# Performance work log

Measured on AMD Instinct MI355X. Metric: run time of the kernel, lower is better.

The kernel has to match this reference:

```python
import jax, jax.numpy as jnp
import numpy as np

MASK_NEG = -1e9

def setup_inputs() -> dict:
    key = jax.random.key(0)
    kq, kk, kv, km = jax.random.split(key, 4)
    B, S, D = 16, 2048, 64
    query = jax.random.normal(kq, (B, S, D), dtype=jnp.float32)
    key_t = jax.random.normal(kk, (B, S, D), dtype=jnp.float32)
    value = jax.random.normal(kv, (B, S, D), dtype=jnp.float32)
    mask = jax.random.randint(km, (B, 1, S), 0, 2, dtype=jnp.int32)
    return {"query": query, "key": key_t, "value": value, "mask": mask}

def reference(query, key, value, mask):
    d = query.shape[-1]
    # scores: [B, S, S]
    scores = jnp.einsum("bqd,bkd->bqk", query, key) / jnp.sqrt(jnp.asarray(d, query.dtype))
    scores = jnp.where(mask == 0, jnp.asarray(MASK_NEG, scores.dtype), scores)
    p_attn = jax.nn.softmax(scores, axis=-1)
    out = jnp.einsum("bqk,bkd->bqd", p_attn, value)
    return out, p_attn
```

## Files before the change

kernel.cpp:

```cpp
#include <hip/hip_runtime.h>
#include <hip/hip_bf16.h>

#define BN 16
#define SN 2048
#define DN 64
#define QB 16
#define NWAVE 8
#define KSEG 256
#define NCH 8

#define SC_L2E 0.18033688011112042f
#define BI_L2E 11.541560327111707f

typedef __attribute__((ext_vector_type(8))) short bf16x8;
typedef __attribute__((ext_vector_type(4))) short bf16x4;
typedef __attribute__((ext_vector_type(4))) float f32x4;
typedef __attribute__((ext_vector_type(4))) int   i32x4;
typedef __attribute__((ext_vector_type(4))) unsigned u32x4;

static __device__ __forceinline__ short f2bf(float f) {
    __hip_bfloat16 h = __float2bfloat16(f);
    union { __hip_bfloat16 h; short s; } u; u.h = h;
    return u.s;
}
static __device__ __forceinline__ float uf(unsigned u) {
    union { unsigned u; float f; } v; v.u = u;
    return v.f;
}
static __device__ __forceinline__ unsigned pk2(float lo, float hi) {
    return ((unsigned)(unsigned short)f2bf(lo)) |
           (((unsigned)(unsigned short)f2bf(hi)) << 16);
}
static __device__ __forceinline__ float fast_exp2(float x) {
#if __has_builtin(__builtin_amdgcn_exp2f)
    return __builtin_amdgcn_exp2f(x);
#else
    return exp2f(x);
#endif
}

__global__ __launch_bounds__(256)
void prep_kv(const float* __restrict__ K, const float* __restrict__ V,
             const int* __restrict__ M,
             short* __restrict__ Kf, short* __restrict__ Vf, float* __restrict__ Mf)
{
    __shared__ short vt[64][72];
    const int b   = blockIdx.x >> 5;
    const int s0  = (blockIdx.x & 31) << 6;
    const int cg0 = s0 >> 5;
    const int tid = threadIdx.x;
    const int sr = tid >> 4;
    const int dc = (tid & 15) << 2;
    #pragma unroll
    for (int i = 0; i < 4; ++i) {
        const int s = sr + i * 16;
        f32x4 vv = *(const f32x4*)(V + ((size_t)b * SN + s0 + s) * DN + dc);
        bf16x4 v4;
        #pragma unroll
        for (int j = 0; j < 4; ++j) v4[j] = f2bf(vv[j]);
        *(bf16x4*)&vt[s][dc] = v4;
    }
    if (tid < 64) {
        const int m = M[(size_t)b * SN + s0 + tid];
        Mf[(size_t)b * SN + s0 + tid] = m ? -BI_L2E : -1e9f;
    }
    __syncthreads();

    #pragma unroll
    for (int r = 0; r < 2; ++r) {
        const int o   = tid + (r << 8);
        const int h   = o >> 8;
        const int s   = (o >> 6) & 3;
        const int l2  = o & 63;
        const int lq2 = l2 & 15, lg2 = l2 >> 4;
        const int srow = s0 + h * 32 + ((s >> 1) & 1) * 16 + lq2;
        const int scol = (s & 1) * 32 + lg2 * 8;
        const float* kp = K + ((size_t)b * SN + srow) * DN + scol;
        f32x4 x = *(const f32x4*)kp;
        f32x4 y = *(const f32x4*)(kp + 4);
        bf16x8 kv;
        #pragma unroll
        for (int j = 0; j < 4; ++j) { kv[j] = f2bf(x[j]); kv[4 + j] = f2bf(y[j]); }
        *(bf16x8*)(Kf + (size_t)(((b * 64 + cg0 + h) * 4 + s) * 512 + l2 * 8)) = kv;
    }
    #pragma unroll
    for (int r = 0; r < 2; ++r) {
        const int o   = tid + (r << 8);
        const int h   = o >> 8;
        const int nt  = (o >> 6) & 3;
        const int l2  = o & 63;
        const int lq2 = l2 & 15, lg2 = l2 >> 4;
        const int d   = nt * 16 + lq2;
        bf16x8 w;
        #pragma unroll
        for (int j = 0; j < 4; ++j) {
            w[j]     = vt[h * 32 + 4 * lg2 + j][d];
            w[4 + j] = vt[h * 32 + 16 + 4 * lg2 + j][d];
        }
        *(bf16x8*)(Vf + (size_t)(((b * 64 + cg0 + h) * 4 + nt) * 512 + l2 * 8)) = w;
    }
}

template <int PRE>
__global__ __launch_bounds__(512, 3)
void attn_fused(const float* __restrict__ Q, const float* __restrict__ K,
                const float* __restrict__ V, const int* __restrict__ M,
                const short* __restrict__ Kf, const short* __restrict__ Vf,
                const float* __restrict__ Mf, float* __restrict__ out)
{
    __shared__ float obuf[NWAVE * QB * DN];
    __shared__ float lred[NWAVE * QB];
    __shared__ float lfin[QB];

    const int tid = threadIdx.x;
    const int wv = tid >> 6, ln = tid & 63;
    const int lq = ln & 15, lg = ln >> 4;

    const int lb = ((blockIdx.x & 7) << 8) | (blockIdx.x >> 3);
    const int bb = lb >> 7;
    const int q0 = (lb & 127) << 4;

    const float* Qb = Q + ((size_t)bb * SN + q0) * DN;
    float* out_o = out + ((size_t)bb * SN + q0) * DN;
    float* out_p = out + (size_t)BN * SN * DN + ((size_t)bb * SN + q0) * SN;

    u32x4* stash = (u32x4*)obuf + (wv << 8) + ln;

    bf16x8 qf0, qf1;
    {
        const float* src = Qb + lq * DN + lg * 8;
        f32x4 a = *(const f32x4*)src;
        f32x4 b = *(const f32x4*)(src + 4);
        f32x4 c = *(const f32x4*)(src + 32);
        f32x4 d = *(const f32x4*)(src + 36);
        #pragma unroll
        for (int j = 0; j < 4; ++j) {
            qf0[j] = f2bf(a[j]); qf0[4 + j] = f2bf(b[j]);
            qf1[j] = f2bf(c[j]); qf1[4 + j] = f2bf(d[j]);
        }
    }

    const int k0 = wv * KSEG;
    const int cgb = bb * 64 + wv * NCH;
    const short* kfp = Kf + (size_t)cgb * 2048 + ln * 8;
    const short* vfp = Vf + (size_t)cgb * 2048 + ln * 8;
    const float* fp  = Mf + (size_t)bb * SN + k0 + 4 * lg;
    const int*   Mb  = M + (size_t)bb * SN;
    const float* Kb  = K + (size_t)bb * SN * DN;
    const float* Vb  = V + (size_t)bb * SN * DN;

    unsigned pk_lo[4][4];
    float ls0 = 0.f, ls1 = 0.f;

    #pragma unroll
    for (int c = 0; c < NCH; ++c) {
        bf16x8 kf0, kf1, kf2, kf3;
        f32x4 b0, b1;
        if constexpr (PRE) {
            kf0 = *(const bf16x8*)(kfp + c * 2048);
            kf1 = *(const bf16x8*)(kfp + c * 2048 + 512);
            kf2 = *(const bf16x8*)(kfp + c * 2048 + 1024);
            kf3 = *(const bf16x8*)(kfp + c * 2048 + 1536);
            b0 = *(const f32x4*)(fp + c * 32);
            b1 = *(const f32x4*)(fp + c * 32 + 16);
        } else {
            const float* ks = Kb + (size_t)(k0 + c * 32 + lq) * DN + lg * 8;
            #pragma unroll
            for (int j = 0; j < 8; ++j) {
                kf0[j] = f2bf(ks[j]);            kf1[j] = f2bf(ks[32 + j]);
                kf2[j] = f2bf(ks[16 * DN + j]);  kf3[j] = f2bf(ks[16 * DN + 32 + j]);
            }
            const i32x4 mv0 = *(const i32x4*)(Mb + k0 + c * 32 + 4 * lg);
            const i32x4 mv1 = *(const i32x4*)(Mb + k0 + c * 32 + 16 + 4 * lg);
            #pragma unroll
            for (int r = 0; r < 4; ++r) {
                b0[r] = mv0[r] ? -BI_L2E : -1e9f;
                b1[r] = mv1[r] ? -BI_L2E : -1e9f;
            }
        }
        f32x4 a0 = {0.f, 0.f, 0.f, 0.f}, a1 = {0.f, 0.f, 0.f, 0.f};
        __builtin_amdgcn_s_setprio(1);
        a0 = __builtin_amdgcn_mfma_f32_16x16x32_bf16(kf0, qf0, a0, 0, 0, 0);
        a0 = __builtin_amdgcn_mfma_f32_16x16x32_bf16(kf1, qf1, a0, 0, 0, 0);
        a1 = __builtin_amdgcn_mfma_f32_16x16x32_bf16(kf2, qf0, a1, 0, 0, 0);
        a1 = __builtin_amdgcn_mfma_f32_16x16x32_bf16(kf3, qf1, a1, 0, 0, 0);

        float p0[4], p1[4];
        #pragma unroll
        for (int r = 0; r < 4; ++r) {
            p0[r] = fast_exp2(fmaf(a0[r], SC_L2E, b0[r]));
            p1[r] = fast_exp2(fmaf(a1[r], SC_L2E, b1[r]));
            ls0 += p0[r];
            ls1 += p1[r];
        }
        u32x4 w;
        w[0] = pk2(p0[0], p0[1]); w[1] = pk2(p0[2], p0[3]);
        w[2] = pk2(p1[0], p1[1]); w[3] = pk2(p1[2], p1[3]);
        __builtin_amdgcn_s_setprio(0);
        if (c < 4) {
            pk_lo[c][0] = w[0]; pk_lo[c][1] = w[1];
            pk_lo[c][2] = w[2]; pk_lo[c][3] = w[3];
        } else {
            stash[(c - 4) << 6] = w;
        }
    }

    bf16x8 pv0[4], pv1[4];
    if constexpr (PRE) {
        pv0[0] = *(const bf16x8*)(vfp);
        pv0[1] = *(const bf16x8*)(vfp + 512);
        pv0[2] = *(const bf16x8*)(vfp + 1024);
        pv0[3] = *(const bf16x8*)(vfp + 1536);
        pv1[0] = *(const bf16x8*)(vfp + 2048);
        pv1[1] = *(const bf16x8*)(vfp + 2048 + 512);
        pv1[2] = *(const bf16x8*)(vfp + 2048 + 1024);
        pv1[3] = *(const bf16x8*)(vfp + 2048 + 1536);
    }

    float lsum = ls0 + ls1;
    lsum += __shfl_xor(lsum, 16);
    lsum += __shfl_xor(lsum, 32);
    if (lg == 0) lred[wv * QB + lq] = lsum;
    __syncthreads();

    float lrow = 0.f;
    #pragma unroll
    for (int w = 0; w < NWAVE; ++w) lrow += lred[w * QB + lq];
    const float rl = 1.f / lrow;
    if (tid < QB) {
        float l = 0.f;
        #pragma unroll
        for (int w = 0; w < NWAVE; ++w) l += lred[w * QB + tid];
        lfin[tid] = 1.f / l;
    }

    f32x4 oacc[4];
    #pragma unroll
    for (int nt = 0; nt < 4; ++nt) oacc[nt] = (f32x4){0.f, 0.f, 0.f, 0.f};
    float* pp = out_p + (size_t)lq * SN + k0 + 4 * lg;

    #pragma unroll
    for (int c = 0; c < NCH; ++c) {
        union { unsigned u[4]; u32x4 w; bf16x8 v; } pa;
        if (c < 4) {
            pa.u[0] = pk_lo[c][0]; pa.u[1] = pk_lo[c][1];
            pa.u[2] = pk_lo[c][2]; pa.u[3] = pk_lo[c][3];
        } else {
            pa.w = stash[(c - 4) << 6];
        }

        f32x4 o0, o1;
        o0[0] = uf(pa.u[0] << 16) * rl;  o0[1] = uf(pa.u[0] & 0xffff0000u) * rl;
        o0[2] = uf(pa.u[1] << 16) * rl;  o0[3] = uf(pa.u[1] & 0xffff0000u) * rl;
        o1[0] = uf(pa.u[2] << 16) * rl;  o1[1] = uf(pa.u[2] & 0xffff0000u) * rl;
        o1[2] = uf(pa.u[3] << 16) * rl;  o1[3] = uf(pa.u[3] & 0xffff0000u) * rl;
        __builtin_nontemporal_store(o0, (f32x4*)(pp + c * 32));
        __builtin_nontemporal_store(o1, (f32x4*)(pp + c * 32 + 16));

        bf16x8 vf0, vf1, vf2, vf3;
        if constexpr (PRE) {
            if (c == 0) { vf0 = pv0[0]; vf1 = pv0[1]; vf2 = pv0[2]; vf3 = pv0[3]; }
            else if (c == 1) { vf0 = pv1[0]; vf1 = pv1[1]; vf2 = pv1[2]; vf3 = pv1[3]; }
            else {
                vf0 = *(const bf16x8*)(vfp + c * 2048);
                vf1 = *(const bf16x8*)(vfp + c * 2048 + 512);
                vf2 = *(const bf16x8*)(vfp + c * 2048 + 1024);
                vf3 = *(const bf16x8*)(vfp + c * 2048 + 1536);
            }
        } else {
            #pragma unroll
            for (int j = 0; j < 4; ++j) {
                const float* va = Vb + (size_t)(k0 + c * 32 + 4 * lg + j) * DN + lq;
                const float* vb = Vb + (size_t)(k0 + c * 32 + 16 + 4 * lg + j) * DN + lq;
                vf0[j] = f2bf(va[0]);  vf0[4 + j] = f2bf(vb[0]);
                vf1[j] = f2bf(va[16]); vf1[4 + j] = f2bf(vb[16]);
                vf2[j] = f2bf(va[32]); vf2[4 + j] = f2bf(vb[32]);
                vf3[j] = f2bf(va[48]); vf3[4 + j] = f2bf(vb[48]);
            }
        }
        __builtin_amdgcn_s_setprio(1);
        oacc[0] = __builtin_amdgcn_mfma_f32_16x16x32_bf16(pa.v, vf0, oacc[0], 0, 0, 0);
        oacc[1] = __builtin_amdgcn_mfma_f32_16x16x32_bf16(pa.v, vf1, oacc[1], 0, 0, 0);
        oacc[2] = __builtin_amdgcn_mfma_f32_16x16x32_bf16(pa.v, vf2, oacc[2], 0, 0, 0);
        oacc[3] = __builtin_amdgcn_mfma_f32_16x16x32_bf16(pa.v, vf3, oacc[3], 0, 0, 0);
        __builtin_amdgcn_s_setprio(0);
    }

    #pragma unroll
    for (int nt = 0; nt < 4; ++nt) {
        #pragma unroll
        for (int r = 0; r < 4; ++r)
            obuf[(wv * QB + 4 * lg + r) * DN + nt * 16 + lq] = oacc[nt][r];
    }
    __syncthreads();
    #pragma unroll
    for (int i = 0; i < 2; ++i) {
        const int idx = tid + i * 512;
        const int q = idx >> 6, d = idx & 63;
        float v = 0.f;
        #pragma unroll
        for (int w = 0; w < NWAVE; ++w) v += obuf[(w * QB + q) * DN + d];
        __builtin_nontemporal_store(v * lfin[q], &out_o[(size_t)q * DN + d]);
    }
}

extern "C" void kernel_launch(void* const* d_in, const int* in_sizes, int n_in,
                              void* d_out, int out_size, void* d_ws, size_t ws_size,
                              hipStream_t stream) {
    const float* Q = (const float*)d_in[0];
    const float* K = (const float*)d_in[1];
    const float* V = (const float*)d_in[2];
    const int*   M = (const int*)d_in[3];
    float* out = (float*)d_out;

    const size_t szKf = (size_t)BN * 64 * 4 * 512 * sizeof(short);
    const size_t szVf = szKf;
    const size_t szMf = (size_t)BN * SN * sizeof(float);
    const size_t need = szKf + szVf + szMf;

    dim3 block(512);
    dim3 grid(BN * (SN / QB));
    if (ws_size >= need) {
        short* Kf = (short*)d_ws;
        short* Vf = (short*)((char*)d_ws + szKf);
        float* Mf = (float*)((char*)d_ws + szKf + szVf);
        prep_kv<<<dim3(BN * (SN / 64)), dim3(256), 0, stream>>>(K, V, M, Kf, Vf, Mf);
        attn_fused<1><<<grid, block, 0, stream>>>(Q, K, V, M, Kf, Vf, Mf, out);
    } else {
        attn_fused<0><<<grid, block, 0, stream>>>(Q, K, V, M, nullptr, nullptr, nullptr, out);
    }
}
```

Baseline: 92.80 us.

## Coalesce attention-probability stores by transposing through LDS stash before writing

Moves the normalized p_attn writes out of the PV MFMA loop. Each wave stashes its packed bf16 probabilities in its LDS slice, then rereads them transposed so 32 lanes write one contiguous 512-byte row segment, instead of 16 scattered 64-byte pieces per store. The per-row reciprocal now comes from the shared lfin array, which needs an extra block barrier. The goal is better write coalescing for the dominant p_attn output traffic, at the cost of extra LDS reads and writes and less overlap between stores and MFMA work.

```diff
diff --git a/kernel.cpp b/kernel.cpp
--- a/kernel.cpp
+++ b/kernel.cpp
@@ -16,6 +16,7 @@
 typedef __attribute__((ext_vector_type(4))) short bf16x4;
 typedef __attribute__((ext_vector_type(4))) float f32x4;
 typedef __attribute__((ext_vector_type(4))) int   i32x4;
+typedef __attribute__((ext_vector_type(2))) unsigned u32x2;
 typedef __attribute__((ext_vector_type(4))) unsigned u32x4;
 
 static __device__ __forceinline__ short f2bf(float f) {
@@ -222,22 +223,17 @@
     lsum += __shfl_xor(lsum, 32);
     if (lg == 0) lred[wv * QB + lq] = lsum;
     __syncthreads();
-
-    float lrow = 0.f;
-    #pragma unroll
-    for (int w = 0; w < NWAVE; ++w) lrow += lred[w * QB + lq];
-    const float rl = 1.f / lrow;
     if (tid < QB) {
         float l = 0.f;
         #pragma unroll
         for (int w = 0; w < NWAVE; ++w) l += lred[w * QB + tid];
         lfin[tid] = 1.f / l;
     }
+    __syncthreads();
 
     f32x4 oacc[4];
     #pragma unroll
     for (int nt = 0; nt < 4; ++nt) oacc[nt] = (f32x4){0.f, 0.f, 0.f, 0.f};
-    float* pp = out_p + (size_t)lq * SN + k0 + 4 * lg;
 
     #pragma unroll
     for (int c = 0; c < NCH; ++c) {
@@ -248,14 +244,6 @@
         } else {
             pa.w = stash[(c - 4) << 6];
         }
-
-        f32x4 o0, o1;
-        o0[0] = uf(pa.u[0] << 16) * rl;  o0[1] = uf(pa.u[0] & 0xffff0000u) * rl;
-        o0[2] = uf(pa.u[1] << 16) * rl;  o0[3] = uf(pa.u[1] & 0xffff0000u) * rl;
-        o1[0] = uf(pa.u[2] << 16) * rl;  o1[1] = uf(pa.u[2] & 0xffff0000u) * rl;
-        o1[2] = uf(pa.u[3] << 16) * rl;  o1[3] = uf(pa.u[3] & 0xffff0000u) * rl;
-        __builtin_nontemporal_store(o0, (f32x4*)(pp + c * 32));
-        __builtin_nontemporal_store(o1, (f32x4*)(pp + c * 32 + 16));
 
         bf16x8 vf0, vf1, vf2, vf3;
         if constexpr (PRE) {
@@ -286,6 +274,45 @@
         __builtin_amdgcn_s_setprio(0);
     }
 
+    {
+        const char* wb = (const char*)obuf + (wv << 12);
+        const int i    = ln & 31;
+        const int c_sl = i >> 3;
+        const int j    = i & 7;
+        const int soff = c_sl * 1024 + ((j & 3) * 16) * 16 + (j >> 2) * 8;
+        const int rsel = ln >> 5;
+
+        #pragma unroll
+        for (int it = 0; it < 8; ++it) {
+            const int row = 2 * it + rsel;
+            const u32x2 w = *(const u32x2*)(wb + soff + row * 16);
+            const float rl = lfin[row];
+            f32x4 o;
+            o[0] = uf(w[0] << 16) * rl;  o[1] = uf(w[0] & 0xffff0000u) * rl;
+            o[2] = uf(w[1] << 16) * rl;  o[3] = uf(w[1] & 0xffff0000u) * rl;
+            __builtin_nontemporal_store(o,
+                (f32x4*)(out_p + (size_t)row * SN + k0 + 128 + i * 4));
+        }
+        #pragma unroll
+        for (int c = 0; c < 4; ++c) {
+            u32x4 w;
+            w[0] = pk_lo[c][0]; w[1] = pk_lo[c][1];
+            w[2] = pk_lo[c][2]; w[3] = pk_lo[c][3];
+            stash[c << 6] = w;
+        }
+        #pragma unroll
+        for (int it = 0; it < 8; ++it) {
+            const int row = 2 * it + rsel;
+            const u32x2 w = *(const u32x2*)(wb + soff + row * 16);
+            const float rl = lfin[row];
+            f32x4 o;
+            o[0] = uf(w[0] << 16) * rl;  o[1] = uf(w[0] & 0xffff0000u) * rl;
+            o[2] = uf(w[1] << 16) * rl;  o[3] = uf(w[1] & 0xffff0000u) * rl;
+            __builtin_nontemporal_store(o,
+                (f32x4*)(out_p + (size_t)row * SN + k0 + i * 4));
+        }
+    }
+
     #pragma unroll
     for (int nt = 0; nt < 4; ++nt) {
         #pragma unroll
```

After: 81.78 us. 1.13x faster.
